# Kernel tuning notes

Hardware: AMD Instinct MI355X
Metric: run time of the kernel (lower is better)

## Reference

```python
import jax, jax.numpy as jnp
import numpy as np

N_HOS, N_TYP, N_STRUCTS = 2, 3, 8
N_COMBOS = N_HOS * N_TYP  # 6
BATCH = 32768
N_ITERS = 150  # PDHG iterations to solve the per-sample QP

S_NP = np.array([[1,0,0,1,0,1,0,0],
                 [0,1,0,1,0,0,1,0],
                 [0,0,1,0,1,0,0,1],
                 [1,0,0,0,1,1,0,0],
                 [0,1,0,0,0,0,1,1],
                 [0,0,1,1,1,0,0,0]], dtype=np.float32)


def setup_inputs() -> dict:
    key = jax.random.key(0)
    ks = jax.random.split(key, 10)
    def lin(kw, fan_in, fan_out):
        lim = 1.0 / np.sqrt(fan_in)
        kw1, kw2 = jax.random.split(kw)
        W = jax.random.uniform(kw1, (fan_out, fan_in), jnp.float32, -lim, lim)
        b = jax.random.uniform(kw2, (fan_out,), jnp.float32, -lim, lim)
        return W, b
    W1, b1 = lin(ks[0], 6, 20)
    W2, b2 = lin(ks[1], 20, 20)
    W3, b3 = lin(ks[2], 20, 20)
    W4, b4 = lin(ks[3], 20, 8)
    X = jax.random.uniform(ks[4], (BATCH, N_HOS, N_TYP), jnp.float32)  # nonneg bids -> feasible QP (x=0)
    return {"X": X, "W1": W1, "b1": b1, "W2": W2, "b2": b2, "W3": W3, "b3": b3,
            "W4": W4, "b4": b4, "S": jnp.asarray(S_NP), "batch_size": BATCH}


def _solve_qp(z, b, S):
    """Batched PDHG for: max w.x - ||x-z||_2  s.t. x>=0, S x <= b, with w = 1.
    z: [B, ns], b: [B, m], S: [m, ns]. Returns x: [B, ns]."""
    B, ns = z.shape
    m = S.shape[0]
    w = jnp.ones_like(z)
    # K = [S; -I]; Frobenius bound on spectral norm (safe step sizes)
    L = jnp.sqrt(jnp.sum(S * S) + ns)
    tau = 0.9 / L
    sigma = 0.9 / L

    def prox_f(u):
        # prox of tau*(||x-z|| - w.x) at u  (closed form: shifted norm shrinkage)
        v = u + tau * w - z
        nv = jnp.linalg.norm(v, axis=-1, keepdims=True)
        scale = jnp.maximum(1.0 - tau / jnp.maximum(nv, 1e-12), 0.0)
        return z + scale * v

    def step(carry, _):
        x, l1, l2 = carry
        x_new = prox_f(x - tau * (l1 @ S - l2))  # K^T lam = S^T l1 - l2
        xbar = 2.0 * x_new - x
        l1n = jnp.maximum(l1 + sigma * (xbar @ S.T) - sigma * b, 0.0)  # dual of Sx<=b
        l2n = jnp.maximum(l2 - sigma * xbar, 0.0)                      # dual of -x<=0
        return (x_new, l1n, l2n), None

    x0 = jnp.maximum(z, 0.0)
    l1 = jnp.zeros((B, m), z.dtype)
    l2 = jnp.zeros((B, ns), z.dtype)
    (x, _, _), _ = jax.lax.scan(step, (x0, l1, l2), None, length=N_ITERS)
    return x


def reference(X, W1, b1, W2, b2, W3, b3, W4, b4, S, batch_size):
    B = X.shape[0]
    Z = X.reshape(B, -1)                       # [B, 6] = bids flattened (also the QP rhs b)
    h = jnp.tanh(Z @ W1.T + b1)
    h = jnp.tanh(h @ W2.T + b2)
    h = jnp.tanh(h @ W3.T + b3)
    z = jnp.tanh(h @ W4.T + b4)                # [B, 8] anchor point for QP
    return _solve_qp(z, Z, S)                  # [B, 8] allocation
```

## Files before the change

kernel.cpp:

```cpp
#include <hip/hip_runtime.h>
#include <math.h>


#define NITERS 150

__device__ __forceinline__ float ftanh(float a) {
    float e = __expf(2.0f * a);
    return fmaf(-2.0f, __builtin_amdgcn_rcpf(e + 1.0f), 1.0f);
}

__global__ __launch_bounds__(64, 1) void matchnet_kernel(
    const float* __restrict__ X,
    const float* __restrict__ W1, const float* __restrict__ b1,
    const float* __restrict__ W2, const float* __restrict__ b2,
    const float* __restrict__ W3, const float* __restrict__ b3,
    const float* __restrict__ W4, const float* __restrict__ b4,
    float* __restrict__ out, int B)
{
    __shared__ float sw[1148];
    const int t = threadIdx.x;
    for (int i = t; i < 120; i += 64) sw[i]        = W1[i];
    for (int i = t; i < 20;  i += 64) sw[120 + i]  = b1[i];
    for (int i = t; i < 400; i += 64) sw[140 + i]  = W2[i];
    for (int i = t; i < 20;  i += 64) sw[540 + i]  = b2[i];
    for (int i = t; i < 400; i += 64) sw[560 + i]  = W3[i];
    for (int i = t; i < 20;  i += 64) sw[960 + i]  = b3[i];
    for (int i = t; i < 160; i += 64) sw[980 + i]  = W4[i];
    if (t < 8) sw[1140 + t] = b4[t];
    __syncthreads();

    const int gid = blockIdx.x * 64 + t;
    if (gid >= B) return;

    const float TAU = 0.9f / sqrtf(26.0f);
    const float SIG = TAU;

    float zin[6];
    {
        const float2* xp = (const float2*)(X + (size_t)gid * 6);
        float2 p0 = xp[0], p1 = xp[1], p2 = xp[2];
        zin[0] = p0.x; zin[1] = p0.y; zin[2] = p1.x;
        zin[3] = p1.y; zin[4] = p2.x; zin[5] = p2.y;
    }

    float h1[20];
#pragma unroll
    for (int j = 0; j < 20; ++j) {
        float a = sw[120 + j];
#pragma unroll
        for (int k = 0; k < 6; ++k) a = fmaf(sw[j*6 + k], zin[k], a);
        h1[j] = ftanh(a);
    }
    float h2[20];
#pragma unroll
    for (int j = 0; j < 20; ++j) {
        float a = sw[540 + j];
#pragma unroll
        for (int k = 0; k < 20; ++k) a = fmaf(sw[140 + j*20 + k], h1[k], a);
        h2[j] = ftanh(a);
    }
    float h3[20];
#pragma unroll
    for (int j = 0; j < 20; ++j) {
        float a = sw[960 + j];
#pragma unroll
        for (int k = 0; k < 20; ++k) a = fmaf(sw[560 + j*20 + k], h2[k], a);
        h3[j] = ftanh(a);
    }
    float z[8];
#pragma unroll
    for (int j = 0; j < 8; ++j) {
        float a = sw[1140 + j];
#pragma unroll
        for (int k = 0; k < 20; ++k) a = fmaf(sw[980 + j*20 + k], h3[k], a);
        z[j] = ftanh(a);
    }

    float xz[8], l2[8];
#pragma unroll
    for (int j = 0; j < 8; ++j) {
        float x0 = fmaxf(z[j], 0.0f);
        xz[j] = x0 - z[j] + TAU;
        l2[j] = 0.0f;
    }
    float l1[6], sb[6];
#pragma unroll
    for (int i = 0; i < 6; ++i) { l1[i] = 0.0f; sb[i] = SIG * zin[i]; }

#pragma unroll 1
    for (int it = 0; it < NITERS; ++it) {
        float t03 = l1[0] + l1[3];
        float t14 = l1[1] + l1[4];
        float t25 = l1[2] + l1[5];
        float st[8];
        st[0] = t03; st[1] = t14; st[2] = t25;
        st[3] = (l1[0] + l1[1]) + l1[5];
        st[4] = (l1[2] + l1[3]) + l1[5];
        st[5] = t03; st[6] = t14;
        st[7] = l1[2] + l1[4];

        float v[8];
#pragma unroll
        for (int j = 0; j < 8; ++j)
            v[j] = fmaf(-TAU, st[j] - l2[j], xz[j]);

        float n01 = fmaf(v[0], v[0], v[1]*v[1]);
        float n23 = fmaf(v[2], v[2], v[3]*v[3]);
        float n45 = fmaf(v[4], v[4], v[5]*v[5]);
        float n67 = fmaf(v[6], v[6], v[7]*v[7]);
        float nv2 = (n01 + n23) + (n45 + n67);
        float scale = fmaxf(fmaf(-TAU, __builtin_amdgcn_rsqf(nv2), 1.0f), 0.0f);

        float xb[8];
#pragma unroll
        for (int j = 0; j < 8; ++j) {
            float sv = scale * v[j];
            float d  = fmaf(2.0f, sv, TAU - xz[j]);
            xz[j] = sv + TAU;
            float xbj = z[j] + d;
            xb[j] = xbj;
            l2[j] = fmaxf(fmaf(-SIG, xbj, l2[j]), 0.0f);
        }

        float r0 = (xb[0] + xb[3]) + xb[5];
        float r1 = (xb[1] + xb[3]) + xb[6];
        float r2 = (xb[2] + xb[4]) + xb[7];
        float r3 = (xb[0] + xb[4]) + xb[5];
        float r4 = (xb[1] + xb[6]) + xb[7];
        float r5 = (xb[2] + xb[3]) + xb[4];
        l1[0] = fmaxf(fmaf(SIG, r0, l1[0]) - sb[0], 0.0f);
        l1[1] = fmaxf(fmaf(SIG, r1, l1[1]) - sb[1], 0.0f);
        l1[2] = fmaxf(fmaf(SIG, r2, l1[2]) - sb[2], 0.0f);
        l1[3] = fmaxf(fmaf(SIG, r3, l1[3]) - sb[3], 0.0f);
        l1[4] = fmaxf(fmaf(SIG, r4, l1[4]) - sb[4], 0.0f);
        l1[5] = fmaxf(fmaf(SIG, r5, l1[5]) - sb[5], 0.0f);
    }

    float x0 = xz[0] + z[0] - TAU, x1 = xz[1] + z[1] - TAU;
    float x2 = xz[2] + z[2] - TAU, x3 = xz[3] + z[3] - TAU;
    float x4 = xz[4] + z[4] - TAU, x5 = xz[5] + z[5] - TAU;
    float x6 = xz[6] + z[6] - TAU, x7 = xz[7] + z[7] - TAU;
    float4* op = (float4*)(out + (size_t)gid * 8);
    op[0] = make_float4(x0, x1, x2, x3);
    op[1] = make_float4(x4, x5, x6, x7);
}

extern "C" void kernel_launch(void* const* d_in, const int* in_sizes, int n_in,
                              void* d_out, int out_size, void* d_ws, size_t ws_size,
                              hipStream_t stream) {
    const float* X  = (const float*)d_in[0];
    const float* W1 = (const float*)d_in[1];
    const float* b1 = (const float*)d_in[2];
    const float* W2 = (const float*)d_in[3];
    const float* b2 = (const float*)d_in[4];
    const float* W3 = (const float*)d_in[5];
    const float* b3 = (const float*)d_in[6];
    const float* W4 = (const float*)d_in[7];
    const float* b4 = (const float*)d_in[8];
    float* out = (float*)d_out;
    const int B = in_sizes[0] / 6;
    const int blocks = (B + 63) / 64;
    hipLaunchKernelGGL(matchnet_kernel, dim3(blocks), dim3(64), 0, stream,
                       X, W1, b1, W2, b2, W3, b3, W4, b4, out, B);
}
```

Before: 124.3 us.

## Read MLP weights from global memory directly and restructure PDHG loop algebra

The LDS staging of the MLP weights and the block barrier are removed. Weights are now read straight from global memory as uniform loads, which the compiler can turn into scalar loads. The PDHG iteration is rewritten algebraically: S·xbar is computed as S·v scaled plus precomputed S·z, and S·x is tracked incrementally, which shortens the per-iteration dependency chain. In exchange there are more live registers and a different floating-point rounding order.

```diff
diff --git a/kernel.cpp b/kernel.cpp
--- a/kernel.cpp
+++ b/kernel.cpp
@@ -17,19 +17,7 @@
     const float* __restrict__ W4, const float* __restrict__ b4,
     float* __restrict__ out, int B)
 {
-    __shared__ float sw[1148];
-    const int t = threadIdx.x;
-    for (int i = t; i < 120; i += 64) sw[i]        = W1[i];
-    for (int i = t; i < 20;  i += 64) sw[120 + i]  = b1[i];
-    for (int i = t; i < 400; i += 64) sw[140 + i]  = W2[i];
-    for (int i = t; i < 20;  i += 64) sw[540 + i]  = b2[i];
-    for (int i = t; i < 400; i += 64) sw[560 + i]  = W3[i];
-    for (int i = t; i < 20;  i += 64) sw[960 + i]  = b3[i];
-    for (int i = t; i < 160; i += 64) sw[980 + i]  = W4[i];
-    if (t < 8) sw[1140 + t] = b4[t];
-    __syncthreads();
-
-    const int gid = blockIdx.x * 64 + t;
+    const int gid = blockIdx.x * 64 + threadIdx.x;
     if (gid >= B) return;
 
     const float TAU = 0.9f / sqrtf(26.0f);
@@ -46,44 +34,62 @@
     float h1[20];
 #pragma unroll
     for (int j = 0; j < 20; ++j) {
-        float a = sw[120 + j];
+        float a = b1[j];
 #pragma unroll
-        for (int k = 0; k < 6; ++k) a = fmaf(sw[j*6 + k], zin[k], a);
+        for (int k = 0; k < 6; ++k) a = fmaf(W1[j*6 + k], zin[k], a);
         h1[j] = ftanh(a);
     }
     float h2[20];
 #pragma unroll
     for (int j = 0; j < 20; ++j) {
-        float a = sw[540 + j];
+        float a = b2[j];
 #pragma unroll
-        for (int k = 0; k < 20; ++k) a = fmaf(sw[140 + j*20 + k], h1[k], a);
+        for (int k = 0; k < 20; ++k) a = fmaf(W2[j*20 + k], h1[k], a);
         h2[j] = ftanh(a);
     }
     float h3[20];
 #pragma unroll
     for (int j = 0; j < 20; ++j) {
-        float a = sw[960 + j];
+        float a = b3[j];
 #pragma unroll
-        for (int k = 0; k < 20; ++k) a = fmaf(sw[560 + j*20 + k], h2[k], a);
+        for (int k = 0; k < 20; ++k) a = fmaf(W3[j*20 + k], h2[k], a);
         h3[j] = ftanh(a);
     }
     float z[8];
 #pragma unroll
     for (int j = 0; j < 8; ++j) {
-        float a = sw[1140 + j];
+        float a = b4[j];
 #pragma unroll
-        for (int k = 0; k < 20; ++k) a = fmaf(sw[980 + j*20 + k], h3[k], a);
+        for (int k = 0; k < 20; ++k) a = fmaf(W4[j*20 + k], h3[k], a);
         z[j] = ftanh(a);
     }
 
-    float xz[8], l2[8];
+    float zpt[8], xz[8], l2[8], p[8];
 #pragma unroll
     for (int j = 0; j < 8; ++j) {
         float x0 = fmaxf(z[j], 0.0f);
         xz[j] = x0 - z[j] + TAU;
+        p[j]  = xz[j];
         l2[j] = 0.0f;
+        zpt[j] = z[j] + TAU;
     }
-    float l1[6], sb[6];
+    float x0_[8];
+#pragma unroll
+    for (int j = 0; j < 8; ++j) x0_[j] = fmaxf(z[j], 0.0f);
+
+    float szc[6], sx[6], sb[6], l1[6];
+    szc[0] = (z[0] + z[3]) + z[5];
+    szc[1] = (z[1] + z[3]) + z[6];
+    szc[2] = (z[2] + z[4]) + z[7];
+    szc[3] = (z[0] + z[4]) + z[5];
+    szc[4] = (z[1] + z[6]) + z[7];
+    szc[5] = (z[2] + z[3]) + z[4];
+    sx[0] = (x0_[0] + x0_[3]) + x0_[5];
+    sx[1] = (x0_[1] + x0_[3]) + x0_[6];
+    sx[2] = (x0_[2] + x0_[4]) + x0_[7];
+    sx[3] = (x0_[0] + x0_[4]) + x0_[5];
+    sx[4] = (x0_[1] + x0_[6]) + x0_[7];
+    sx[5] = (x0_[2] + x0_[3]) + x0_[4];
 #pragma unroll
     for (int i = 0; i < 6; ++i) { l1[i] = 0.0f; sb[i] = SIG * zin[i]; }
 
@@ -101,8 +107,19 @@
 
         float v[8];
 #pragma unroll
-        for (int j = 0; j < 8; ++j)
-            v[j] = fmaf(-TAU, st[j] - l2[j], xz[j]);
+        for (int j = 0; j < 8; ++j) v[j] = fmaf(-TAU, st[j], p[j]);
+
+        float zx[8];
+#pragma unroll
+        for (int j = 0; j < 8; ++j) zx[j] = zpt[j] - xz[j];
+
+        float sv[6];
+        sv[0] = (v[0] + v[3]) + v[5];
+        sv[1] = (v[1] + v[3]) + v[6];
+        sv[2] = (v[2] + v[4]) + v[7];
+        sv[3] = (v[0] + v[4]) + v[5];
+        sv[4] = (v[1] + v[6]) + v[7];
+        sv[5] = (v[2] + v[3]) + v[4];
 
         float n01 = fmaf(v[0], v[0], v[1]*v[1]);
         float n23 = fmaf(v[2], v[2], v[3]*v[3]);
@@ -110,39 +127,31 @@
         float n67 = fmaf(v[6], v[6], v[7]*v[7]);
         float nv2 = (n01 + n23) + (n45 + n67);
         float scale = fmaxf(fmaf(-TAU, __builtin_amdgcn_rsqf(nv2), 1.0f), 0.0f);
+        float ss2 = scale + scale;
 
-        float xb[8];
 #pragma unroll
         for (int j = 0; j < 8; ++j) {
-            float sv = scale * v[j];
-            float d  = fmaf(2.0f, sv, TAU - xz[j]);
-            xz[j] = sv + TAU;
-            float xbj = z[j] + d;
-            xb[j] = xbj;
+            float xbj = fmaf(ss2, v[j], zx[j]);
+            xz[j] = fmaf(scale, v[j], TAU);
             l2[j] = fmaxf(fmaf(-SIG, xbj, l2[j]), 0.0f);
+            p[j]  = fmaf(TAU, l2[j], xz[j]);
         }
 
-        float r0 = (xb[0] + xb[3]) + xb[5];
-        float r1 = (xb[1] + xb[3]) + xb[6];
-        float r2 = (xb[2] + xb[4]) + xb[7];
-        float r3 = (xb[0] + xb[4]) + xb[5];
-        float r4 = (xb[1] + xb[6]) + xb[7];
-        float r5 = (xb[2] + xb[3]) + xb[4];
-        l1[0] = fmaxf(fmaf(SIG, r0, l1[0]) - sb[0], 0.0f);
-        l1[1] = fmaxf(fmaf(SIG, r1, l1[1]) - sb[1], 0.0f);
-        l1[2] = fmaxf(fmaf(SIG, r2, l1[2]) - sb[2], 0.0f);
-        l1[3] = fmaxf(fmaf(SIG, r3, l1[3]) - sb[3], 0.0f);
-        l1[4] = fmaxf(fmaf(SIG, r4, l1[4]) - sb[4], 0.0f);
-        l1[5] = fmaxf(fmaf(SIG, r5, l1[5]) - sb[5], 0.0f);
+#pragma unroll
+        for (int i = 0; i < 6; ++i) {
+            float sxn = fmaf(scale, sv[i], szc[i]);
+            float d   = fmaf(2.0f, sxn, -sx[i]);
+            sx[i] = sxn;
+            l1[i] = fmaxf(fmaf(SIG, d, l1[i]) - sb[i], 0.0f);
+        }
     }
 
-    float x0 = xz[0] + z[0] - TAU, x1 = xz[1] + z[1] - TAU;
-    float x2 = xz[2] + z[2] - TAU, x3 = xz[3] + z[3] - TAU;
-    float x4 = xz[4] + z[4] - TAU, x5 = xz[5] + z[5] - TAU;
-    float x6 = xz[6] + z[6] - TAU, x7 = xz[7] + z[7] - TAU;
+    const float T2 = 2.0f * TAU;
     float4* op = (float4*)(out + (size_t)gid * 8);
-    op[0] = make_float4(x0, x1, x2, x3);
-    op[1] = make_float4(x4, x5, x6, x7);
+    op[0] = make_float4(xz[0] + zpt[0] - T2, xz[1] + zpt[1] - T2,
+                        xz[2] + zpt[2] - T2, xz[3] + zpt[3] - T2);
+    op[1] = make_float4(xz[4] + zpt[4] - T2, xz[5] + zpt[5] - T2,
+                        xz[6] + zpt[6] - T2, xz[7] + zpt[7] - T2);
 }
 
 extern "C" void kernel_launch(void* const* d_in, const int* in_sizes, int n_in,
```

Result: no change. 121.9 us (-1.9%).
